# Performance work log

Measured on AMD Instinct MI355X. Metric: run time of the kernel, lower is better.

The kernel has to match this reference:

```python
import jax, jax.numpy as jnp
import numpy as np

N = 100000
E = 600000
D = 128          # in_channels
D_OUT = 128      # out_channels


def setup_inputs() -> dict:
    key = jax.random.key(0)
    ks = jax.random.split(key, 8)
    node_embeddings = jax.random.normal(ks[0], (N, D), dtype=jnp.float32)
    edge_index = jax.random.randint(ks[1], (2, E), 0, N, dtype=jnp.int64)
    s = 1.0 / np.sqrt(D)
    W_src = jax.random.uniform(ks[2], (D, D), minval=-s, maxval=s, dtype=jnp.float32)
    W_tgt = jax.random.uniform(ks[3], (D, D), minval=-s, maxval=s, dtype=jnp.float32)
    s2 = 1.0 / np.sqrt(2 * D)
    W_proj = jax.random.uniform(ks[4], (2 * D, D_OUT), minval=-s2, maxval=s2, dtype=jnp.float32)
    b_proj = jax.random.uniform(ks[5], (D_OUT,), minval=-s2, maxval=s2, dtype=jnp.float32)
    s3 = 1.0 / np.sqrt(D_OUT)
    W_mlp = jax.random.uniform(ks[6], (D_OUT, D_OUT), minval=-s3, maxval=s3, dtype=jnp.float32)
    b_mlp = jax.random.uniform(ks[7], (D_OUT,), minval=-s3, maxval=s3, dtype=jnp.float32)
    return {
        "node_embeddings": node_embeddings,
        "edge_index": edge_index,
        "W_src": W_src,
        "W_tgt": W_tgt,
        "W_proj": W_proj,
        "b_proj": b_proj,
        "W_mlp": W_mlp,
        "b_mlp": b_mlp,
    }


def reference(node_embeddings, edge_index, W_src, W_tgt, W_proj, b_proj, W_mlp, b_mlp):
    src = node_embeddings[edge_index[0]]   # [E, D]
    tgt = node_embeddings[edge_index[1]]   # [E, D]
    gate_s = jax.nn.sigmoid(src @ W_src)   # Linear no bias + sigmoid
    gate_t = jax.nn.sigmoid(tgt @ W_tgt)
    attn_s = gate_s * src
    attn_t = gate_t * tgt
    edge_attr = jnp.concatenate([attn_s, attn_t], axis=-1)  # [E, 2D]
    edge_attr = edge_attr @ W_proj + b_proj                  # [E, D_OUT]
    return jax.nn.relu(edge_attr) @ W_mlp + b_mlp
```

## Files before the change

### kernel.cpp

```cpp
#include <hip/hip_runtime.h>

#define NN 100000
#define NE 600000
#define DD 128

typedef _Float16 half4_t __attribute__((ext_vector_type(4)));
typedef _Float16 half8_t __attribute__((ext_vector_type(8)));
typedef float f32x4 __attribute__((ext_vector_type(4)));

__device__ __forceinline__ int swzb(int row, int byte) {
  return row * 256 + (byte ^ ((row & 7) << 4));
}

__device__ __forceinline__ half8_t relu_add(half8_t a, half8_t b) {
  half8_t r;
#pragma unroll
  for (int j = 0; j < 8; ++j) {
    const _Float16 s = a[j] + b[j];
    r[j] = s > (_Float16)0 ? s : (_Float16)0;
  }
  return r;
}

__global__ void prep_kernel(const float* __restrict__ Wsrc,
                            const float* __restrict__ Wtgt,
                            const float* __restrict__ Wproj,
                            const float* __restrict__ Wmlp,
                            const unsigned int* __restrict__ eraw,
                            int* __restrict__ idx,
                            _Float16* __restrict__ packed) {
  const int bid = (int)blockIdx.x;
  const int tid = (int)threadIdx.x;
  if (bid < 40) {
    const int t = bid * 256 + tid;
    if (t >= 5 * 2048) return;
    const int m = t >> 11;
    const int rem = t & 2047;
    const int nf = rem >> 8;
    const int ks = (rem >> 6) & 3;
    const int l = rem & 63;
    const float* W;
    if (m == 0) W = Wsrc;
    else if (m == 1) W = Wtgt;
    else if (m == 2) W = Wproj;
    else if (m == 3) W = Wproj + 128 * DD;
    else W = Wmlp;
    const int col = (l & 15) + 16 * nf;
    const int k0 = 8 * (l >> 4) + 32 * ks;
    half8_t v;
#pragma unroll
    for (int j = 0; j < 8; ++j)
      v[j] = (_Float16)W[(size_t)(k0 + j) * DD + col];
    *reinterpret_cast<half8_t*>(packed + (size_t)m * 16384 +
                                (size_t)rem * 8) = v;
  } else {
    __shared__ int s_is64;
    if (tid < 64) {
      const unsigned long long b = __ballot(eraw[2 * tid + 1] != 0u);
      if (tid == 0) s_is64 = (b == 0ull) ? 1 : 0;
    }
    __syncthreads();
    const int is64 = s_is64;
    const size_t stride = (size_t)512 * 256;
    for (size_t i = (size_t)(bid - 40) * 256 + tid; i < 2 * (size_t)NE;
         i += stride)
      idx[i] = (int)(is64 ? eraw[2 * i] : eraw[i]);
  }
}

__global__ __launch_bounds__(256, 4)
void phase1_kernel(const float* __restrict__ Xg,
                   const _Float16* __restrict__ packW,
                   const float* __restrict__ bproj,
                   _Float16* __restrict__ Aout,
                   _Float16* __restrict__ Bout) {
  __shared__ _Float16 Xh[64 * DD];
  __shared__ _Float16 Th[64 * DD];
  const int tid = (int)threadIdx.x;
  const int row0 = (int)blockIdx.x * 64;
  const int rem = NN - row0;
  const int nvalid = rem < 64 ? rem : 64;

#pragma unroll
  for (int it = 0; it < 8; ++it) {
    const int i = tid + it * 256;
    const int r = i >> 5;
    const int c4 = i & 31;
    float4 v = make_float4(0.f, 0.f, 0.f, 0.f);
    if (r < nvalid)
      v = reinterpret_cast<const float4*>(Xg + (size_t)(row0 + r) * DD)[c4];
    half4_t h;
    h[0] = (_Float16)v.x; h[1] = (_Float16)v.y;
    h[2] = (_Float16)v.z; h[3] = (_Float16)v.w;
    *reinterpret_cast<half4_t*>(&Xh[swzb(r, c4 * 8) >> 1]) = h;
  }
  __syncthreads();

  const int l = tid & 63;
  const int w = tid >> 6;
  const int lr = l & 15;
  const int lg = l >> 4;

#pragma unroll 1
  for (int p = 0; p < 2; ++p) {
    const _Float16* __restrict__ wb1 = packW + (size_t)p * 16384 + l * 8;
    half8_t w1[2][4];
#pragma unroll
    for (int s = 0; s < 2; ++s)
#pragma unroll
      for (int ks = 0; ks < 4; ++ks)
        w1[s][ks] = *reinterpret_cast<const half8_t*>(
            wb1 + (size_t)(((2 * w + s) * 4 + ks)) * 512);

    f32x4 acc[4][2];
#pragma unroll
    for (int mf = 0; mf < 4; ++mf)
#pragma unroll
      for (int s = 0; s < 2; ++s) acc[mf][s] = (f32x4)0.f;
#pragma unroll
    for (int mf = 0; mf < 4; ++mf) {
      half8_t xf[4];
#pragma unroll
      for (int ks = 0; ks < 4; ++ks)
        xf[ks] = *reinterpret_cast<const half8_t*>(
            &Xh[swzb(mf * 16 + lr, lg * 16 + ks * 64) >> 1]);
#pragma unroll
      for (int ks = 0; ks < 4; ++ks)
#pragma unroll
        for (int s = 0; s < 2; ++s)
          acc[mf][s] = __builtin_amdgcn_mfma_f32_16x16x32_f16(
              w1[s][ks], xf[ks], acc[mf][s], 0, 0, 0);
    }

    if (p) __syncthreads();

#pragma unroll
    for (int mf = 0; mf < 4; ++mf)
#pragma unroll
      for (int s = 0; s < 2; ++s) {
        const int c0 = (2 * w + s) * 16 + lg * 4;
        const int node = mf * 16 + lr;
        const half4_t xh =
            *reinterpret_cast<const half4_t*>(&Xh[swzb(node, c0 * 2) >> 1]);
        half4_t th;
#pragma unroll
        for (int j = 0; j < 4; ++j) {
          const float t = (float)xh[j] / (1.f + __expf(-acc[mf][s][j]));
          th[j] = (_Float16)t;
        }
        *reinterpret_cast<half4_t*>(&Th[swzb(node, c0 * 2) >> 1]) = th;
      }
    __syncthreads();

    const _Float16* __restrict__ wb2 = packW + (size_t)(2 + p) * 16384 + l * 8;
    half8_t w2[2][4];
#pragma unroll
    for (int s = 0; s < 2; ++s)
#pragma unroll
      for (int ks = 0; ks < 4; ++ks)
        w2[s][ks] = *reinterpret_cast<const half8_t*>(
            wb2 + (size_t)(((2 * w + s) * 4 + ks)) * 512);

    f32x4 acc2[4][2];
#pragma unroll
    for (int mf = 0; mf < 4; ++mf)
#pragma unroll
      for (int s = 0; s < 2; ++s) acc2[mf][s] = (f32x4)0.f;
#pragma unroll
    for (int mf = 0; mf < 4; ++mf) {
      half8_t tf[4];
#pragma unroll
      for (int ks = 0; ks < 4; ++ks)
        tf[ks] = *reinterpret_cast<const half8_t*>(
            &Th[swzb(mf * 16 + lr, lg * 16 + ks * 64) >> 1]);
#pragma unroll
      for (int ks = 0; ks < 4; ++ks)
#pragma unroll
        for (int s = 0; s < 2; ++s)
          acc2[mf][s] = __builtin_amdgcn_mfma_f32_16x16x32_f16(
              w2[s][ks], tf[ks], acc2[mf][s], 0, 0, 0);
    }

    _Float16* __restrict__ dst = p ? Bout : Aout;
#pragma unroll
    for (int s = 0; s < 2; ++s) {
      const int c0 = (2 * w + s) * 16 + lg * 4;
      f32x4 bp = (f32x4)0.f;
      if (p == 0) bp = *reinterpret_cast<const f32x4*>(bproj + c0);
#pragma unroll
      for (int mf = 0; mf < 4; ++mf) {
        const int node = mf * 16 + lr;
        if (node < nvalid) {
          const f32x4 v = acc2[mf][s] + bp;
          half4_t h;
#pragma unroll
          for (int j = 0; j < 4; ++j) h[j] = (_Float16)v[j];
          *reinterpret_cast<half4_t*>(dst + (size_t)(row0 + node) * DD + c0) =
              h;
        }
      }
    }
  }
}

__global__ __launch_bounds__(256, 5)
void phase2_kernel(const _Float16* __restrict__ At,
                   const _Float16* __restrict__ Bt,
                   const int* __restrict__ idx,
                   const _Float16* __restrict__ Wpk,
                   const float* __restrict__ bmlp,
                   float* __restrict__ out) {
  __shared__ _Float16 Wl[16384];
  const int tid = (int)threadIdx.x;
  const int l = tid & 63;
  const int w = tid >> 6;
  const int lr = l & 15;
  const int lg = l >> 4;
  const int er = (int)blockIdx.x * 64 + w * 16 + lr;

  const int ia = idx[er];
  const int ib = idx[(size_t)NE + er];
  const _Float16* __restrict__ pa = At + (size_t)ia * DD + lg * 8;
  const _Float16* __restrict__ pb = Bt + (size_t)ib * DD + lg * 8;
  half8_t af[4], bf[4];
#pragma unroll
  for (int ks = 0; ks < 4; ++ks) {
    af[ks] = *reinterpret_cast<const half8_t*>(pa + ks * 32);
    bf[ks] = *reinterpret_cast<const half8_t*>(pb + ks * 32);
  }

#pragma unroll
  for (int i = 0; i < 8; ++i) {
    const int c = tid + i * 256;
    reinterpret_cast<f32x4*>(Wl)[c] = reinterpret_cast<const f32x4*>(Wpk)[c];
  }

  f32x4 acc[8];
#pragma unroll
  for (int nf = 0; nf < 8; ++nf) acc[nf] = (f32x4)0.f;

  __syncthreads();

#pragma unroll
  for (int ks = 0; ks < 4; ++ks) {
    const half8_t r = relu_add(af[ks], bf[ks]);
#pragma unroll
    for (int nf = 0; nf < 8; ++nf) {
      const half8_t wf = *reinterpret_cast<const half8_t*>(
          &Wl[(size_t)(nf * 4 + ks) * 512 + l * 8]);
      acc[nf] =
          __builtin_amdgcn_mfma_f32_16x16x32_f16(wf, r, acc[nf], 0, 0, 0);
    }
  }

#pragma unroll
  for (int nf = 0; nf < 8; ++nf) {
    const int c0 = nf * 16 + lg * 4;
    const f32x4 bm = *reinterpret_cast<const f32x4*>(bmlp + c0);
    const f32x4 v = acc[nf] + bm;
    __builtin_nontemporal_store(
        v, reinterpret_cast<f32x4*>(out + (size_t)er * DD + c0));
  }
}

extern "C" void kernel_launch(void* const* d_in, const int* in_sizes, int n_in,
                              void* d_out, int out_size, void* d_ws,
                              size_t ws_size, hipStream_t stream) {
  (void)in_sizes; (void)n_in; (void)out_size; (void)ws_size;

  const float* X = (const float*)d_in[0];
  const unsigned int* eraw = (const unsigned int*)d_in[1];
  const float* Wsrc = (const float*)d_in[2];
  const float* Wtgt = (const float*)d_in[3];
  const float* Wproj = (const float*)d_in[4];
  const float* bproj = (const float*)d_in[5];
  const float* Wmlp = (const float*)d_in[6];
  const float* bmlp = (const float*)d_in[7];
  float* out = (float*)d_out;

  _Float16* A16 = (_Float16*)d_ws;
  _Float16* B16 = A16 + (size_t)NN * DD;
  _Float16* packW = B16 + (size_t)NN * DD;
  int* idx = (int*)(packW + 5 * 16384);

  prep_kernel<<<552, 256, 0, stream>>>(Wsrc, Wtgt, Wproj, Wmlp, eraw, idx,
                                       packW);
  phase1_kernel<<<(NN + 63) / 64, 256, 0, stream>>>(X, packW, bproj, A16, B16);
  phase2_kernel<<<NE / 64, 256, 0, stream>>>(A16, B16, idx,
                                             packW + 4 * 16384, bmlp, out);
}
```

Before: 173.7 us.

## Bucket-sort edges by source node to improve gather locality in phase2

Adds a histogram, scan and scatter pass that groups edges into coarse buckets by source node (512-node buckets), storing sorted source, target and original edge ids. Phase2 reads edges in this bucketed order, spread over 8 interleaved chunks, so source-row gathers hit L2 more often, and writes each output row back to its original edge slot. This adds three small kernels plus extra index traffic, and turns the output writes into scattered stores, which may cost more than the gather locality saves.

```diff
diff --git a/kernel.cpp b/kernel.cpp
--- a/kernel.cpp
+++ b/kernel.cpp
@@ -3,6 +3,9 @@
 #define NN 100000
 #define NE 600000
 #define DD 128
+#define NB 196
+#define CHUNK 75000
+#define BPC 1172
 
 typedef _Float16 half4_t __attribute__((ext_vector_type(4)));
 typedef _Float16 half8_t __attribute__((ext_vector_type(8)));
@@ -20,6 +23,10 @@
     r[j] = s > (_Float16)0 ? s : (_Float16)0;
   }
   return r;
+}
+
+__global__ void zero_kernel(int* __restrict__ hist) {
+  if (threadIdx.x < NB) hist[threadIdx.x] = 0;
 }
 
 __global__ void prep_kernel(const float* __restrict__ Wsrc,
@@ -28,6 +35,7 @@
                             const float* __restrict__ Wmlp,
                             const unsigned int* __restrict__ eraw,
                             int* __restrict__ idx,
+                            int* __restrict__ hist,
                             _Float16* __restrict__ packed) {
   const int bid = (int)blockIdx.x;
   const int tid = (int)threadIdx.x;
@@ -55,6 +63,8 @@
                                 (size_t)rem * 8) = v;
   } else {
     __shared__ int s_is64;
+    __shared__ int lh[NB];
+    if (tid < NB) lh[tid] = 0;
     if (tid < 64) {
       const unsigned long long b = __ballot(eraw[2 * tid + 1] != 0u);
       if (tid == 0) s_is64 = (b == 0ull) ? 1 : 0;
@@ -63,8 +73,69 @@
     const int is64 = s_is64;
     const size_t stride = (size_t)512 * 256;
     for (size_t i = (size_t)(bid - 40) * 256 + tid; i < 2 * (size_t)NE;
-         i += stride)
-      idx[i] = (int)(is64 ? eraw[2 * i] : eraw[i]);
+         i += stride) {
+      const int v = (int)(is64 ? eraw[2 * i] : eraw[i]);
+      idx[i] = v;
+      if (i < (size_t)NE) atomicAdd(&lh[v >> 9], 1);
+    }
+    __syncthreads();
+    if (tid < NB && lh[tid]) atomicAdd(&hist[tid], lh[tid]);
+  }
+}
+
+__global__ void scan_kernel(const int* __restrict__ hist,
+                            int* __restrict__ cursor) {
+  if (threadIdx.x == 0 && blockIdx.x == 0) {
+    int acc = 0;
+#pragma unroll 1
+    for (int b = 0; b < NB; ++b) {
+      cursor[b] = acc;
+      acc += hist[b];
+    }
+  }
+}
+
+__global__ __launch_bounds__(256)
+void scatter_kernel(const int* __restrict__ idx, int* __restrict__ cursor,
+                    int* __restrict__ sortedS, int* __restrict__ sortedT,
+                    int* __restrict__ sortedE) {
+  __shared__ int lh[NB];
+  __shared__ int lbase[NB];
+  const int tid = (int)threadIdx.x;
+  const int e0 = (int)blockIdx.x * 1024;
+  if (tid < NB) lh[tid] = 0;
+  __syncthreads();
+
+  int sv[4], tv[4], bv[4];
+  bool val[4];
+#pragma unroll
+  for (int k = 0; k < 4; ++k) {
+    const int e = e0 + tid + k * 256;
+    val[k] = e < NE;
+    if (val[k]) {
+      sv[k] = idx[e];
+      tv[k] = idx[(size_t)NE + e];
+      bv[k] = sv[k] >> 9;
+      atomicAdd(&lh[bv[k]], 1);
+    }
+  }
+  __syncthreads();
+  if (tid < NB) {
+    const int c = lh[tid];
+    lbase[tid] = c ? atomicAdd(&cursor[tid], c) : 0;
+  }
+  __syncthreads();
+  if (tid < NB) lh[tid] = 0;
+  __syncthreads();
+#pragma unroll
+  for (int k = 0; k < 4; ++k) {
+    if (val[k]) {
+      const int r = atomicAdd(&lh[bv[k]], 1);
+      const int pos = lbase[bv[k]] + r;
+      sortedS[pos] = sv[k];
+      sortedT[pos] = tv[k];
+      sortedE[pos] = e0 + tid + k * 256;
+    }
   }
 }
 
@@ -206,7 +277,9 @@
 __global__ __launch_bounds__(256, 5)
 void phase2_kernel(const _Float16* __restrict__ At,
                    const _Float16* __restrict__ Bt,
-                   const int* __restrict__ idx,
+                   const int* __restrict__ sortedS,
+                   const int* __restrict__ sortedT,
+                   const int* __restrict__ sortedE,
                    const _Float16* __restrict__ Wpk,
                    const float* __restrict__ bmlp,
                    float* __restrict__ out) {
@@ -216,10 +289,15 @@
   const int w = tid >> 6;
   const int lr = l & 15;
   const int lg = l >> 4;
-  const int er = (int)blockIdx.x * 64 + w * 16 + lr;
-
-  const int ia = idx[er];
-  const int ib = idx[(size_t)NE + er];
+  const int bid = (int)blockIdx.x;
+  const int base = (bid & 7) * CHUNK;
+  const int loc = (bid >> 3) * 64 + w * 16 + lr;
+  const bool valid = loc < CHUNK;
+  const int g = base + (valid ? loc : 0);
+
+  const int ia = sortedS[g];
+  const int ib = sortedT[g];
+  const int eo = sortedE[g];
   const _Float16* __restrict__ pa = At + (size_t)ia * DD + lg * 8;
   const _Float16* __restrict__ pb = Bt + (size_t)ib * DD + lg * 8;
   half8_t af[4], bf[4];
@@ -258,8 +336,9 @@
     const int c0 = nf * 16 + lg * 4;
     const f32x4 bm = *reinterpret_cast<const f32x4*>(bmlp + c0);
     const f32x4 v = acc[nf] + bm;
-    __builtin_nontemporal_store(
-        v, reinterpret_cast<f32x4*>(out + (size_t)er * DD + c0));
+    if (valid)
+      __builtin_nontemporal_store(
+          v, reinterpret_cast<f32x4*>(out + (size_t)eo * DD + c0));
   }
 }
 
@@ -282,10 +361,20 @@
   _Float16* B16 = A16 + (size_t)NN * DD;
   _Float16* packW = B16 + (size_t)NN * DD;
   int* idx = (int*)(packW + 5 * 16384);
-
+  int* hist = idx + 2 * (size_t)NE;
+  int* cursor = hist + NB;
+  int* sortedS = cursor + NB;
+  int* sortedT = sortedS + NE;
+  int* sortedE = sortedT + NE;
+
+  zero_kernel<<<1, 256, 0, stream>>>(hist);
   prep_kernel<<<552, 256, 0, stream>>>(Wsrc, Wtgt, Wproj, Wmlp, eraw, idx,
-                                       packW);
+                                       hist, packW);
+  scan_kernel<<<1, 64, 0, stream>>>(hist, cursor);
+  scatter_kernel<<<(NE + 1023) / 1024, 256, 0, stream>>>(idx, cursor, sortedS,
+                                                         sortedT, sortedE);
   phase1_kernel<<<(NN + 63) / 64, 256, 0, stream>>>(X, packW, bproj, A16, B16);
-  phase2_kernel<<<NE / 64, 256, 0, stream>>>(A16, B16, idx,
-                                             packW + 4 * 16384, bmlp, out);
-}
+  phase2_kernel<<<8 * BPC, 256, 0, stream>>>(A16, B16, sortedS, sortedT,
+                                             sortedE, packW + 4 * 16384, bmlp,
+                                             out);
+}
```

Result: slower. 203.2 us (+17.0%).
